# Kernel tuning notes

Measured on AMD Instinct MI355X. Metric: run time of the kernel, lower is better.

Reference implementation:

```python
import jax, jax.numpy as jnp
import numpy as np

N_SAMPLES = 20000
N_PROPS = 128      # max_radial * n_species = 16 * 8
N_COMBINED = 256
N_ANGULAR = 6      # max_angular + 1


def setup_inputs() -> dict:
    key = jax.random.key(0)
    ks = jax.random.split(key, N_ANGULAR + 1)
    inp = {}
    for l in range(N_ANGULAR):
        # block values: [n_samples, 2l+1 components, n_properties]
        inp[f"values_l{l}"] = jax.random.normal(ks[l], (N_SAMPLES, 2 * l + 1, N_PROPS), dtype=jnp.float32)
    # learned combining matrix, torch.rand -> uniform[0,1)
    inp["W"] = jax.random.uniform(ks[N_ANGULAR], (N_ANGULAR, N_PROPS, N_COMBINED), dtype=jnp.float32)
    return inp


def reference(values_l0, values_l1, values_l2, values_l3, values_l4, values_l5, W):
    blocks = [values_l0, values_l1, values_l2, values_l3, values_l4, values_l5]
    # Per-angular-order GEMM: [s, m, p] @ [p, c] -> [s, m, c], flattened and
    # concatenated over blocks so the ragged output is a single array.
    outs = [
        jnp.einsum("smp,pc->smc", v, W[l]).reshape(-1, W.shape[-1])
        for l, v in enumerate(blocks)
    ]
    return jnp.concatenate(outs, axis=0)  # [sum_l n_samples*(2l+1), n_combined]
```

## Files before the change

### kernel.cpp

```cpp
#include <hip/hip_runtime.h>
#include <hip/hip_bf16.h>

typedef __attribute__((ext_vector_type(8))) short bf16x8;
typedef __attribute__((ext_vector_type(4))) float f32x4;

__device__ __forceinline__ short f2bf(float f) {
    __hip_bfloat16 h = __float2bfloat16(f);
    return *reinterpret_cast<short*>(&h);
}

__global__ void __launch_bounds__(256) combine_mfma_kernel(
    const float* __restrict__ A0, const float* __restrict__ A1,
    const float* __restrict__ A2, const float* __restrict__ A3,
    const float* __restrict__ A4, const float* __restrict__ A5,
    const float* __restrict__ W, float* __restrict__ out)
{
    int b = (int)blockIdx.x;
    int l, boff;
    if      (b <   79) { l = 0; boff = 0;    }
    else if (b <  314) { l = 1; boff = 79;   }
    else if (b <  705) { l = 2; boff = 314;  }
    else if (b < 1252) { l = 3; boff = 705;  }
    else if (b < 1956) { l = 4; boff = 1252; }
    else               { l = 5; boff = 1956; }
    const float* A = (l==0)?A0:(l==1)?A1:(l==2)?A2:(l==3)?A3:(l==4)?A4:A5;
    const int rows = 20000 * (2*l + 1);
    const int row_start = (b - boff) * 256;
    const int ntiles = min(256, rows - row_start) >> 4;
    const size_t outbase = (size_t)20000 * l * l;

    const int tid  = (int)threadIdx.x;
    const int lane = tid & 63;
    const int wv   = tid >> 6;
    const int lr   = lane & 15;
    const int lk   = lane >> 4;

    __shared__ float smem[4096];

    const float* Wl = W + (size_t)l * 128 * 256;
    bf16x8 bfrag[4][4];
    #pragma unroll
    for (int kf = 0; kf < 4; ++kf) {
        const int k0 = kf*32 + lk*8;
        #pragma unroll
        for (int nf = 0; nf < 4; ++nf) {
            const int col = wv*64 + nf*16 + lr;
            bf16x8 t;
            #pragma unroll
            for (int j = 0; j < 8; ++j)
                t[j] = f2bf(Wl[(size_t)(k0 + j)*256 + col]);
            bfrag[kf][nf] = t;
        }
    }

    const char* Abase = (const char*)A + (size_t)row_start * 512;

    auto stage = [&](int t, int buf) {
        const char* tb = Abase + (size_t)t * 8192;
        #pragma unroll
        for (int j = 0; j < 2; ++j) {
            const int lin = wv*2048 + j*1024 + lane*16;
            const int src = lin ^ (((lin >> 9) & 7) << 4);
            __builtin_amdgcn_global_load_lds(
                (const __attribute__((address_space(1))) void*)(tb + src),
                (__attribute__((address_space(3))) void*)
                    ((char*)smem + buf*8192 + wv*2048 + j*1024),
                16, 0, 0);
        }
    };

    auto load_frags = [&](int buf, bf16x8* af) {
        const char* base = (const char*)smem + buf*8192;
        const int sw = (lr & 7) << 4;
        #pragma unroll
        for (int kf = 0; kf < 4; ++kf) {
            const int G0 = lr*512 + kf*128 + lk*32;
            f32x4 x = *(const f32x4*)(base + (G0 ^ sw));
            f32x4 y = *(const f32x4*)(base + ((G0 + 16) ^ sw));
            bf16x8 a;
            a[0]=f2bf(x[0]); a[1]=f2bf(x[1]); a[2]=f2bf(x[2]); a[3]=f2bf(x[3]);
            a[4]=f2bf(y[0]); a[5]=f2bf(y[1]); a[6]=f2bf(y[2]); a[7]=f2bf(y[3]);
            af[kf] = a;
        }
    };

    stage(0, 0);
    asm volatile("s_waitcnt vmcnt(0)" ::: "memory");
    __builtin_amdgcn_s_barrier();

    for (int t = 0; t < ntiles; ++t) {
        bf16x8 af[4];
        load_frags(t & 1, af);

        if (t + 1 < ntiles) stage(t + 1, (t + 1) & 1);

        f32x4 acc[4] = {{0.f,0.f,0.f,0.f},{0.f,0.f,0.f,0.f},
                        {0.f,0.f,0.f,0.f},{0.f,0.f,0.f,0.f}};
        #pragma unroll
        for (int kf = 0; kf < 4; ++kf)
            #pragma unroll
            for (int nf = 0; nf < 4; ++nf)
                acc[nf] = __builtin_amdgcn_mfma_f32_16x16x32_bf16(
                    bfrag[kf][nf], af[kf], acc[nf], 0, 0, 0);

        const int m0 = row_start + t*16;
        float* orow = out + (outbase + (size_t)m0 + lr) * 256 + wv*64 + lk*4;
        #pragma unroll
        for (int nf = 0; nf < 4; ++nf)
            *(f32x4*)(orow + nf*16) = acc[nf];

        if (t + 1 < ntiles) {
            asm volatile("s_waitcnt vmcnt(4)" ::: "memory");
            __builtin_amdgcn_s_barrier();
        }
    }
}

extern "C" void kernel_launch(void* const* d_in, const int* in_sizes, int n_in,
                              void* d_out, int out_size, void* d_ws, size_t ws_size,
                              hipStream_t stream) {
    (void)in_sizes; (void)n_in; (void)out_size; (void)d_ws; (void)ws_size;
    combine_mfma_kernel<<<dim3(2816), dim3(256), 0, stream>>>(
        (const float*)d_in[0], (const float*)d_in[1], (const float*)d_in[2],
        (const float*)d_in[3], (const float*)d_in[4], (const float*)d_in[5],
        (const float*)d_in[6], (float*)d_out);
}
```

Measured before the change: 231.9 us.

## Give each wave a private LDS double buffer and remove block barriers

Each of the four waves now stages the whole 16-row A tile into its own 16 KB double buffer with global_load_lds, and waits only on its own vmcnt instead of a block-wide s_barrier. Staging of the next tile is issued before the current one is computed, so waves run their pipelines independently. The goal is to remove barrier stalls between waves. In exchange, every A tile is fetched four times through L2, and LDS per block grows to 64 KB, which lowers how many blocks fit on a CU.

```diff
diff --git a/kernel.cpp b/kernel.cpp
--- a/kernel.cpp
+++ b/kernel.cpp
@@ -35,7 +35,8 @@
     const int lr   = lane & 15;
     const int lk   = lane >> 4;
 
-    __shared__ float smem[4096];
+    __shared__ char smem[65536];
+    char* mybuf = smem + wv * 16384;
 
     const float* Wl = W + (size_t)l * 128 * 256;
     bf16x8 bfrag[4][4];
@@ -55,23 +56,24 @@
 
     const char* Abase = (const char*)A + (size_t)row_start * 512;
 
-    auto stage = [&](int t, int buf) {
-        const char* tb = Abase + (size_t)t * 8192;
+    auto stage = [&](int T, int buf) {
+        const char* tb = Abase + (size_t)T * 8192;
         #pragma unroll
-        for (int j = 0; j < 2; ++j) {
-            const int lin = wv*2048 + j*1024 + lane*16;
+        for (int j = 0; j < 8; ++j) {
+            const int lin = j*1024 + lane*16;
             const int src = lin ^ (((lin >> 9) & 7) << 4);
             __builtin_amdgcn_global_load_lds(
                 (const __attribute__((address_space(1))) void*)(tb + src),
                 (__attribute__((address_space(3))) void*)
-                    ((char*)smem + buf*8192 + wv*2048 + j*1024),
+                    (mybuf + buf*8192 + j*1024),
                 16, 0, 0);
         }
     };
 
-    auto load_frags = [&](int buf, bf16x8* af) {
-        const char* base = (const char*)smem + buf*8192;
+    auto run_tile = [&](int T, int buf) {
+        const char* base = mybuf + buf*8192;
         const int sw = (lr & 7) << 4;
+        bf16x8 af[4];
         #pragma unroll
         for (int kf = 0; kf < 4; ++kf) {
             const int G0 = lr*512 + kf*128 + lk*32;
@@ -82,18 +84,6 @@
             a[4]=f2bf(y[0]); a[5]=f2bf(y[1]); a[6]=f2bf(y[2]); a[7]=f2bf(y[3]);
             af[kf] = a;
         }
-    };
-
-    stage(0, 0);
-    asm volatile("s_waitcnt vmcnt(0)" ::: "memory");
-    __builtin_amdgcn_s_barrier();
-
-    for (int t = 0; t < ntiles; ++t) {
-        bf16x8 af[4];
-        load_frags(t & 1, af);
-
-        if (t + 1 < ntiles) stage(t + 1, (t + 1) & 1);
-
         f32x4 acc[4] = {{0.f,0.f,0.f,0.f},{0.f,0.f,0.f,0.f},
                         {0.f,0.f,0.f,0.f},{0.f,0.f,0.f,0.f}};
         #pragma unroll
@@ -102,17 +92,28 @@
             for (int nf = 0; nf < 4; ++nf)
                 acc[nf] = __builtin_amdgcn_mfma_f32_16x16x32_bf16(
                     bfrag[kf][nf], af[kf], acc[nf], 0, 0, 0);
-
-        const int m0 = row_start + t*16;
+        const int m0 = row_start + T*16;
         float* orow = out + (outbase + (size_t)m0 + lr) * 256 + wv*64 + lk*4;
         #pragma unroll
         for (int nf = 0; nf < 4; ++nf)
             *(f32x4*)(orow + nf*16) = acc[nf];
+    };
 
-        if (t + 1 < ntiles) {
-            asm volatile("s_waitcnt vmcnt(4)" ::: "memory");
-            __builtin_amdgcn_s_barrier();
+    stage(0, 0);
+    for (int T = 0; T < ntiles; ++T) {
+        const int buf = T & 1;
+        const bool more = (T + 1 < ntiles);
+        if (more) stage(T + 1, buf ^ 1);
+
+        if (T == 0) {
+            if (more) asm volatile("s_waitcnt vmcnt(8)"  ::: "memory");
+            else      asm volatile("s_waitcnt vmcnt(0)"  ::: "memory");
+        } else {
+            if (more) asm volatile("s_waitcnt vmcnt(12)" ::: "memory");
+            else      asm volatile("s_waitcnt vmcnt(4)"  ::: "memory");
         }
+
+        run_tile(T, buf);
     }
 }
 
```

Result: slower. 278.6 us (+20.1%).
